# Kernel tuning notes

Hardware: AMD Instinct MI355X
Metric: run time of the kernel (lower is better)

## Reference

```python
import jax, jax.numpy as jnp
import numpy as np

D_MODEL = 1024
HIDDEN = 2048
D_STATE = 16
KERN = 3
BATCH = 2
SEQ = 2048


def _layernorm(x, g, b, eps=1e-5):
    m = jnp.mean(x, axis=-1, keepdims=True)
    v = jnp.var(x, axis=-1, keepdims=True)
    return (x - m) * jax.lax.rsqrt(v + eps) * g + b


def setup_inputs() -> dict:
    key = jax.random.key(0)
    ks = jax.random.split(key, 10)
    w_scale = 0.02  # keep pre-activations in a sane range (mimics trained-net init)
    return {
        "x": jax.random.normal(ks[0], (BATCH, SEQ, D_MODEL), jnp.float32),
        "W_x": jax.random.normal(ks[1], (HIDDEN, D_MODEL), jnp.float32) * w_scale,
        "b_x": jnp.zeros((HIDDEN,), jnp.float32),
        "W_g": jax.random.normal(ks[2], (HIDDEN, D_MODEL), jnp.float32) * w_scale,
        "b_g": jnp.zeros((HIDDEN,), jnp.float32),
        "conv_w": jax.random.normal(ks[3], (HIDDEN, 1, KERN), jnp.float32) * 0.3,
        "conv_b": jnp.zeros((HIDDEN,), jnp.float32),
        "A_raw": jax.random.normal(ks[4], (HIDDEN, D_STATE), jnp.float32),
        "B_ssm": jax.random.normal(ks[5], (HIDDEN, D_STATE), jnp.float32),
        "C_ssm": jax.random.normal(ks[6], (HIDDEN, D_STATE), jnp.float32),
        "W_dt": jax.random.normal(ks[7], (HIDDEN, D_MODEL), jnp.float32) * w_scale,
        "b_dt": jnp.zeros((HIDDEN,), jnp.float32),
        "W_out": jax.random.normal(ks[8], (D_MODEL, HIDDEN), jnp.float32) * w_scale,
        "b_out": jnp.zeros((D_MODEL,), jnp.float32),
        "ln_g": jnp.ones((D_MODEL,), jnp.float32),
        "ln_b": jnp.zeros((D_MODEL,), jnp.float32),
    }


def reference(x, W_x, b_x, W_g, b_g, conv_w, conv_b, A_raw, B_ssm, C_ssm,
              W_dt, b_dt, W_out, b_out, ln_g, ln_b):
    # projections: u, gate
    u = jnp.einsum('bld,hd->blh', x, W_x) + b_x                    # [B,L,H]
    g = jax.nn.sigmoid(jnp.einsum('bld,hd->blh', x, W_g) + b_g)    # [B,L,H]
    # depthwise conv over time (padding = kernel//2, 'same' for odd kernel)
    pad = conv_w.shape[-1] // 2
    h = jax.lax.conv_general_dilated(
        jnp.transpose(u, (0, 2, 1)), conv_w,
        window_strides=(1,), padding=[(pad, pad)],
        feature_group_count=conv_w.shape[0],
        dimension_numbers=('NCH', 'OIH', 'NCH')) + conv_b[None, :, None]
    h = jnp.transpose(h, (0, 2, 1))                                # [B,L,H]
    u = u * g + h * (1.0 - g)
    # time-invariant dt per channel (mean over batch & time, clamped)
    dt = jax.nn.softplus(jnp.einsum('bld,hd->blh', x, W_dt) + b_dt).mean(axis=(0, 1))
    dt = jnp.clip(dt, 1e-3, 2.0)                                   # [H]
    # discretize
    A = -jax.nn.softplus(A_raw)                                    # [H,S]
    A_d = jnp.exp(A * dt[:, None])                                 # [H,S]
    B_d = (A_d - 1.0) / (A + 1e-6) * B_ssm                         # [H,S]
    # selective scan: state s[b,h,k] = A_d*s + B_d*u_t ; y = <s, C>
    Bsz, L, H = u.shape
    S = A_d.shape[1]

    def step(carry, u_t):                                          # u_t: [B,H]
        new = A_d[None] * carry + B_d[None] * u_t[:, :, None]      # [B,H,S]
        y_t = jnp.einsum('bhs,hs->bh', new, C_ssm)
        return new, y_t

    init = jnp.zeros((Bsz, H, S), dtype=u.dtype)
    _, ys = jax.lax.scan(step, init, jnp.transpose(u, (1, 0, 2)))  # ys: [L,B,H]
    y = jnp.transpose(ys, (1, 0, 2))                               # [B,L,H]
    out = jnp.einsum('blh,dh->bld', y, W_out) + b_out
    return _layernorm(x + out, ln_g, ln_b)
```

## Files before the change

### kernel.cpp

```cpp
#include <hip/hip_runtime.h>
#include <math.h>

#define D_MODEL 1024
#define HIDDEN  2048
#define D_STATE 16
#define BATCH   2
#define SEQ     2048
#define NTOK    (BATCH*SEQ)
#define CHUNK   64
#define NCHUNK  (SEQ/CHUNK)

typedef __attribute__((ext_vector_type(8))) short bf16x8;
typedef __attribute__((ext_vector_type(8))) unsigned short ushort8;
typedef __attribute__((ext_vector_type(4))) float f32x4;

#define GLOAD_LDS16(gptr, lptr) \
    __builtin_amdgcn_global_load_lds((const __attribute__((address_space(1))) void*)(gptr), \
                                     (__attribute__((address_space(3))) void*)(lptr), 16, 0, 0)

__device__ __forceinline__ float softplus_f(float x) {
    return fmaxf(x, 0.0f) + log1pf(expf(-fabsf(x)));
}
__device__ __forceinline__ float sigmoid_f(float x) {
    return 1.0f / (1.0f + expf(-x));
}
__device__ __forceinline__ ushort f2bf(float f) {
    unsigned u = __float_as_uint(f);
    unsigned r = (u + 0x7fffu + ((u >> 16) & 1u)) >> 16;
    return (ushort)r;
}
__device__ __forceinline__ float bf2f(ushort u) {
    return __uint_as_float(((unsigned)u) << 16);
}

__global__ __launch_bounds__(256) void cvt_all(
    const float* __restrict__ x, const float* __restrict__ Wx,
    const float* __restrict__ Wg, const float* __restrict__ Wdt,
    const float* __restrict__ Wout, ushort* __restrict__ arena)
{
    int i = blockIdx.x * 256 + threadIdx.x;
    const float* src; int base;
    if      (i < 1048576) { src = x;    base = 0; }
    else if (i < 1572864) { src = Wx;   base = 1048576; }
    else if (i < 2097152) { src = Wg;   base = 1572864; }
    else if (i < 2621440) { src = Wdt;  base = 2097152; }
    else                  { src = Wout; base = 2621440; }
    float4 v = reinterpret_cast<const float4*>(src)[i - base];
    ushort4 o = { f2bf(v.x), f2bf(v.y), f2bf(v.z), f2bf(v.w) };
    reinterpret_cast<ushort4*>(arena)[i] = o;
}

__device__ __forceinline__ void kloop_pipe3(
    const ushort* __restrict__ A, const ushort* __restrict__ B,
    int K, int m0, int n0, ushort* As, ushort* Bs,
    f32x4 (&acc)[4][4], int lane, int w, int wm, int wn)
{
    const int lr   = lane >> 2;
    const int kc   = (lane & 3) * 8;
    const int quad = lane >> 4;
    const int fr   = lane & 15;

    const int slab0 = w * 2;
    const int r0 = slab0 * 16 + lr;
    const int r1 = r0 + 16;
    const size_t ga0 = (size_t)(m0 + r0) * K + kc;
    const size_t ga1 = (size_t)(m0 + r1) * K + kc;
    const size_t gb0 = (size_t)(n0 + r0) * K + kc;
    const size_t gb1 = (size_t)(n0 + r1) * K + kc;

    const int niter = K / 32;
    GLOAD_LDS16(A + ga0,      &As[slab0 * 512]);
    GLOAD_LDS16(A + ga1,      &As[slab0 * 512 + 512]);
    GLOAD_LDS16(B + gb0,      &Bs[slab0 * 512]);
    GLOAD_LDS16(B + gb1,      &Bs[slab0 * 512 + 512]);
    GLOAD_LDS16(A + ga0 + 32, &As[4096 + slab0 * 512]);
    GLOAD_LDS16(A + ga1 + 32, &As[4096 + slab0 * 512 + 512]);
    GLOAD_LDS16(B + gb0 + 32, &Bs[4096 + slab0 * 512]);
    GLOAD_LDS16(B + gb1 + 32, &Bs[4096 + slab0 * 512 + 512]);

    int buf = 0;
    for (int i = 0; i < niter; i++) {
        asm volatile("s_waitcnt vmcnt(4) lgkmcnt(0)" ::: "memory");
        asm volatile("s_barrier" ::: "memory");
        int nb = buf + 2; if (nb >= 3) nb -= 3;
        const size_t koff = (i + 2 < niter) ? (size_t)(i + 2) * 32 : 0;
        GLOAD_LDS16(A + ga0 + koff, &As[nb * 4096 + slab0 * 512]);
        GLOAD_LDS16(A + ga1 + koff, &As[nb * 4096 + slab0 * 512 + 512]);
        GLOAD_LDS16(B + gb0 + koff, &Bs[nb * 4096 + slab0 * 512]);
        GLOAD_LDS16(B + gb1 + koff, &Bs[nb * 4096 + slab0 * 512 + 512]);

        const ushort* as = &As[buf * 4096];
        const ushort* bs = &Bs[buf * 4096];
        bf16x8 af[4], bfv[4];
        #pragma unroll
        for (int t = 0; t < 4; t++) {
            af[t]  = *reinterpret_cast<const bf16x8*>(&as[(wm * 64 + t * 16 + fr) * 32 + quad * 8]);
            bfv[t] = *reinterpret_cast<const bf16x8*>(&bs[(wn * 64 + t * 16 + fr) * 32 + quad * 8]);
        }
        #pragma unroll
        for (int ii = 0; ii < 4; ii++)
            #pragma unroll
            for (int jj = 0; jj < 4; jj++)
                acc[ii][jj] = __builtin_amdgcn_mfma_f32_16x16x32_bf16(af[ii], bfv[jj], acc[ii][jj], 0, 0, 0);
        buf = (buf == 2) ? 0 : buf + 1;
    }
    asm volatile("s_waitcnt vmcnt(0) lgkmcnt(0)" ::: "memory");
    asm volatile("s_barrier" ::: "memory");
}

__global__ __launch_bounds__(256) void proj_gemm_fused(
    const ushort* __restrict__ xbf, const ushort* __restrict__ Wcat,
    const float* __restrict__ b_x, const float* __restrict__ b_g,
    const float* __restrict__ b_dt, ushort* __restrict__ u_out,
    ushort* __restrict__ g_out, float* __restrict__ dt_sum)
{
    __shared__ ushort S[24576];
    ushort* As = S;
    ushort* Bs = S + 12288;
    const int tid = threadIdx.x, lane = tid & 63, w = tid >> 6;
    const int wm = w & 1, wn = w >> 1;
    const int m0 = blockIdx.x * 128, n0 = blockIdx.y * 128;
    const int quad = lane >> 4, fr = lane & 15;

    f32x4 acc[4][4];
    #pragma unroll
    for (int i = 0; i < 4; i++)
        #pragma unroll
        for (int j = 0; j < 4; j++)
            acc[i][j] = (f32x4){0.f, 0.f, 0.f, 0.f};

    kloop_pipe3(xbf, Wcat, D_MODEL, m0, n0, As, Bs, acc, lane, w, wm, wn);

    const int region = n0 >> 11;
    const int ncb = n0 & 2047;

    if (region == 2) {
        #pragma unroll
        for (int j = 0; j < 4; j++) {
            int n = ncb + wn * 64 + j * 16 + fr;
            float bj = b_dt[n];
            float s = 0.f;
            #pragma unroll
            for (int i = 0; i < 4; i++)
                #pragma unroll
                for (int r = 0; r < 4; r++)
                    s += softplus_f(acc[i][j][r] + bj);
            s += __shfl_xor(s, 16);
            s += __shfl_xor(s, 32);
            if (lane < 16) atomicAdd(&dt_sum[n], s);
        }
    } else {
        const float* bias = region ? b_g : b_x;
        ushort* out = region ? g_out : u_out;
        ushort* Cs = S;
        #pragma unroll
        for (int j = 0; j < 4; j++) {
            int col = wn * 64 + j * 16 + fr;
            float bj = bias[ncb + col];
            #pragma unroll
            for (int i = 0; i < 4; i++) {
                int row = wm * 64 + i * 16 + quad * 4;
                #pragma unroll
                for (int r = 0; r < 4; r++) {
                    float v = acc[i][j][r] + bj;
                    if (region) v = sigmoid_f(v);
                    Cs[(row + r) * 128 + col] = f2bf(v);
                }
            }
        }
        __syncthreads();
        #pragma unroll
        for (int k = 0; k < 8; k++) {
            int v = k * 256 + tid;
            int row = v >> 4, c = (v & 15) * 8;
            *reinterpret_cast<ushort8*>(&out[(size_t)(m0 + row) * HIDDEN + ncb + c]) =
                *reinterpret_cast<const ushort8*>(&Cs[v * 8]);
        }
    }
}

__global__ __launch_bounds__(256) void gemm_out(
    const ushort* __restrict__ ybf, const ushort* __restrict__ Wout,
    const float* __restrict__ b_out, const float* __restrict__ x,
    float* __restrict__ resid)
{
    __shared__ ushort S[24576];
    ushort* As = S;
    ushort* Bs = S + 12288;
    const int tid = threadIdx.x, lane = tid & 63, w = tid >> 6;
    const int wm = w & 1, wn = w >> 1;
    const int m0 = blockIdx.x * 128, n0 = blockIdx.y * 128;
    const int quad = lane >> 4, fr = lane & 15;

    f32x4 acc[4][4];
    #pragma unroll
    for (int i = 0; i < 4; i++)
        #pragma unroll
        for (int j = 0; j < 4; j++)
            acc[i][j] = (f32x4){0.f, 0.f, 0.f, 0.f};

    kloop_pipe3(ybf, Wout, HIDDEN, m0, n0, As, Bs, acc, lane, w, wm, wn);

    float* Sf = (float*)S;
    #pragma unroll
    for (int phase = 0; phase < 2; phase++) {
        if (wm == phase) {
            #pragma unroll
            for (int j = 0; j < 4; j++) {
                int col = wn * 64 + j * 16 + fr;
                float bj = b_out[n0 + col];
                #pragma unroll
                for (int i = 0; i < 4; i++) {
                    int row = i * 16 + quad * 4;
                    #pragma unroll
                    for (int r = 0; r < 4; r++)
                        Sf[(row + r) * 128 + col] = acc[i][j][r] + bj;
                }
            }
        }
        __syncthreads();
        #pragma unroll
        for (int k = 0; k < 8; k++) {
            int v = k * 256 + tid;
            int row = v >> 5, c = (v & 31) * 4;
            size_t off = (size_t)(m0 + phase * 64 + row) * D_MODEL + n0 + c;
            float4 xa = *reinterpret_cast<const float4*>(&x[off]);
            float4 cv = *reinterpret_cast<const float4*>(&Sf[v * 4]);
            float4 o = { cv.x + xa.x, cv.y + xa.y, cv.z + xa.z, cv.w + xa.w };
            *reinterpret_cast<float4*>(&resid[off]) = o;
        }
        __syncthreads();
    }
}

__global__ __launch_bounds__(256) void dt_finalize(
    const float* __restrict__ dt_sum, const float* __restrict__ A_raw,
    const float* __restrict__ B_ssm, float* __restrict__ A_d,
    float* __restrict__ B_d, float* __restrict__ A_dL)
{
    int i = blockIdx.x * 256 + threadIdx.x;
    if (i >= HIDDEN * D_STATE) return;
    int h = i >> 4;
    float dt = dt_sum[h] * (1.0f / NTOK);
    dt = fminf(fmaxf(dt, 1e-3f), 2.0f);
    float Av = -softplus_f(A_raw[i]);
    float Ad = expf(Av * dt);
    float Bd = (Ad - 1.0f) / (Av + 1e-6f) * B_ssm[i];
    A_d[i] = Ad;
    B_d[i] = Bd;
    A_dL[i] = expf(Av * dt * CHUNK);
}

__global__ __launch_bounds__(256) void scan_pass1(
    const ushort* __restrict__ u_bf, const ushort* __restrict__ g_bf,
    const float* __restrict__ conv_w, const float* __restrict__ conv_b,
    const float* __restrict__ A_d, const float* __restrict__ B_d,
    const float* __restrict__ C_ssm,
    ushort* __restrict__ ypart, float* __restrict__ states)
{
    int idx = blockIdx.x * 256 + threadIdx.x;
    int h  = idx & (HIDDEN - 1);
    int bc = idx >> 11;
    int c  = bc & (NCHUNK - 1);
    int b  = bc >> 5;
    float Ad[D_STATE], Bd[D_STATE], Cv[D_STATE], st[D_STATE];
    const float4* a4 = reinterpret_cast<const float4*>(A_d  + h * D_STATE);
    const float4* b4 = reinterpret_cast<const float4*>(B_d  + h * D_STATE);
    const float4* c4 = reinterpret_cast<const float4*>(C_ssm + h * D_STATE);
    #pragma unroll
    for (int q = 0; q < 4; q++) {
        float4 av = a4[q], bv = b4[q], cv = c4[q];
        Ad[q*4+0]=av.x; Ad[q*4+1]=av.y; Ad[q*4+2]=av.z; Ad[q*4+3]=av.w;
        Bd[q*4+0]=bv.x; Bd[q*4+1]=bv.y; Bd[q*4+2]=bv.z; Bd[q*4+3]=bv.w;
        Cv[q*4+0]=cv.x; Cv[q*4+1]=cv.y; Cv[q*4+2]=cv.z; Cv[q*4+3]=cv.w;
    }
    #pragma unroll
    for (int s = 0; s < D_STATE; s++) st[s] = 0.f;

    float w0 = conv_w[h * 3 + 0], w1 = conv_w[h * 3 + 1];
    float w2 = conv_w[h * 3 + 2], cb = conv_b[h];
    const int tok0 = c * CHUNK;
    const size_t base = ((size_t)b * SEQ + tok0) * HIDDEN + h;
    float u_prev = (tok0 > 0) ? bf2f(u_bf[base - HIDDEN]) : 0.f;
    float u_cur  = bf2f(u_bf[base]);
    for (int l = 0; l < CHUNK; l++) {
        float u_next = (tok0 + l + 1 < SEQ) ? bf2f(u_bf[base + (size_t)(l + 1) * HIDDEN]) : 0.f;
        float gv = bf2f(g_bf[base + (size_t)l * HIDDEN]);
        float conv = u_prev * w0 + u_cur * w1 + u_next * w2 + cb;
        float uv = u_cur * gv + conv * (1.0f - gv);
        float y0 = 0.f, y1 = 0.f, y2 = 0.f, y3 = 0.f;
        #pragma unroll
        for (int s = 0; s < D_STATE; s += 4) {
            st[s+0] = fmaf(Ad[s+0], st[s+0], Bd[s+0] * uv);
            st[s+1] = fmaf(Ad[s+1], st[s+1], Bd[s+1] * uv);
            st[s+2] = fmaf(Ad[s+2], st[s+2], Bd[s+2] * uv);
            st[s+3] = fmaf(Ad[s+3], st[s+3], Bd[s+3] * uv);
            y0 = fmaf(st[s+0], Cv[s+0], y0);
            y1 = fmaf(st[s+1], Cv[s+1], y1);
            y2 = fmaf(st[s+2], Cv[s+2], y2);
            y3 = fmaf(st[s+3], Cv[s+3], y3);
        }
        ypart[base + (size_t)l * HIDDEN] = f2bf((y0 + y1) + (y2 + y3));
        u_prev = u_cur; u_cur = u_next;
    }
    float4* sp = reinterpret_cast<float4*>(states + ((size_t)bc * HIDDEN + h) * D_STATE);
    #pragma unroll
    for (int q = 0; q < 4; q++)
        sp[q] = (float4){st[q*4+0], st[q*4+1], st[q*4+2], st[q*4+3]};
}

__global__ __launch_bounds__(256) void scan_pass2(
    float* __restrict__ states, const float* __restrict__ A_dL)
{
    int idx = blockIdx.x * 256 + threadIdx.x;
    int s = idx & 15;
    int h = (idx >> 4) & (HIDDEN - 1);
    int b = idx >> 15;
    float aL = A_dL[h * D_STATE + s];
    float carry = 0.f;
    for (int c = 0; c < NCHUNK; c++) {
        size_t addr = (((size_t)(b * NCHUNK + c) * HIDDEN) + h) * D_STATE + s;
        float fin = states[addr];
        states[addr] = carry;
        carry = fmaf(aL, carry, fin);
    }
}

__global__ __launch_bounds__(256) void scan_pass3(
    const ushort* __restrict__ ypart, const float* __restrict__ states,
    const float* __restrict__ A_d, const float* __restrict__ C_ssm,
    ushort* __restrict__ ybf)
{
    int idx = blockIdx.x * 256 + threadIdx.x;
    int h  = idx & (HIDDEN - 1);
    int bc = idx >> 11;
    int c  = bc & (NCHUNK - 1);
    int b  = bc >> 5;
    float Ad[D_STATE], t[D_STATE];
    const float* sp = states + ((size_t)bc * HIDDEN + h) * D_STATE;
    #pragma unroll
    for (int s = 0; s < D_STATE; s++) {
        float a = A_d[h * D_STATE + s];
        Ad[s] = a;
        t[s] = C_ssm[h * D_STATE + s] * a * sp[s];
    }
    const size_t base = ((size_t)b * SEQ + (size_t)c * CHUNK) * HIDDEN + h;
    for (int l = 0; l < CHUNK; l++) {
        float c0 = 0.f, c1 = 0.f;
        #pragma unroll
        for (int s = 0; s < D_STATE; s += 2) {
            c0 += t[s];
            c1 += t[s + 1];
            t[s] *= Ad[s];
            t[s + 1] *= Ad[s + 1];
        }
        ybf[base + (size_t)l * HIDDEN] = f2bf(bf2f(ypart[base + (size_t)l * HIDDEN]) + (c0 + c1));
    }
}

__global__ __launch_bounds__(256) void ln_kernel(
    const float* __restrict__ resid, const float* __restrict__ ln_g,
    const float* __restrict__ ln_b, float* __restrict__ out)
{
    int row = blockIdx.x;
    int tid = threadIdx.x;
    const float4 v = reinterpret_cast<const float4*>(resid + (size_t)row * D_MODEL)[tid];
    float s  = v.x + v.y + v.z + v.w;
    float ss = v.x * v.x + v.y * v.y + v.z * v.z + v.w * v.w;
    #pragma unroll
    for (int off = 32; off > 0; off >>= 1) {
        s  += __shfl_down(s, off);
        ss += __shfl_down(ss, off);
    }
    __shared__ float sbuf[4], ssbuf[4];
    int wid = tid >> 6, lane = tid & 63;
    if (lane == 0) { sbuf[wid] = s; ssbuf[wid] = ss; }
    __syncthreads();
    float tot  = sbuf[0] + sbuf[1] + sbuf[2] + sbuf[3];
    float tot2 = ssbuf[0] + ssbuf[1] + ssbuf[2] + ssbuf[3];
    float mean = tot * (1.0f / D_MODEL);
    float var  = tot2 * (1.0f / D_MODEL) - mean * mean;
    float rstd = rsqrtf(var + 1e-5f);
    const float4 gv = reinterpret_cast<const float4*>(ln_g)[tid];
    const float4 bv = reinterpret_cast<const float4*>(ln_b)[tid];
    float4 o;
    o.x = (v.x - mean) * rstd * gv.x + bv.x;
    o.y = (v.y - mean) * rstd * gv.y + bv.y;
    o.z = (v.z - mean) * rstd * gv.z + bv.z;
    o.w = (v.w - mean) * rstd * gv.w + bv.w;
    reinterpret_cast<float4*>(out + (size_t)row * D_MODEL)[tid] = o;
}

extern "C" void kernel_launch(void* const* d_in, const int* in_sizes, int n_in,
                              void* d_out, int out_size, void* d_ws, size_t ws_size,
                              hipStream_t stream) {
    const float* x      = (const float*)d_in[0];
    const float* W_x    = (const float*)d_in[1];
    const float* b_x    = (const float*)d_in[2];
    const float* W_g    = (const float*)d_in[3];
    const float* b_g    = (const float*)d_in[4];
    const float* conv_w = (const float*)d_in[5];
    const float* conv_b = (const float*)d_in[6];
    const float* A_raw  = (const float*)d_in[7];
    const float* B_ssm  = (const float*)d_in[8];
    const float* C_ssm  = (const float*)d_in[9];
    const float* W_dt   = (const float*)d_in[10];
    const float* b_dt   = (const float*)d_in[11];
    const float* W_out  = (const float*)d_in[12];
    const float* b_out  = (const float*)d_in[13];
    const float* ln_g   = (const float*)d_in[14];
    const float* ln_b   = (const float*)d_in[15];

    char* W = (char*)d_ws;
    ushort* arena   = (ushort*)(W);
    ushort* x_bf    = arena;
    ushort* Wcat    = arena + 4194304;
    ushort* Wout_bf = arena + 10485760;
    ushort* u_bf    = (ushort*)(W + (24ull << 20));
    ushort* g_bf    = (ushort*)(W + (40ull << 20));
    ushort* ypart   = (ushort*)(W + (56ull << 20));
    float*  resid   = (float*)(W + (40ull << 20));
    float*  states  = (float*)(W + (72ull << 20));
    float*  dt_sum  = (float*)(W + (80ull << 20));
    float*  A_d     = (float*)(W + (80ull << 20) + 65536);
    float*  B_d     = (float*)(W + (80ull << 20) + 65536 + 131072);
    float*  A_dL    = (float*)(W + (80ull << 20) + 65536 + 262144);
    ushort* y_bf    = u_bf;

    hipMemsetAsync(dt_sum, 0, HIDDEN * sizeof(float), stream);

    dim3 blk(256);
    cvt_all<<<12288, blk, 0, stream>>>(x, W_x, W_g, W_dt, W_out, arena);

    dim3 grid_proj(NTOK / 128, 3 * HIDDEN / 128);
    proj_gemm_fused<<<grid_proj, blk, 0, stream>>>(x_bf, Wcat, b_x, b_g, b_dt,
                                                   u_bf, g_bf, dt_sum);
    dt_finalize<<<(HIDDEN * D_STATE) / 256, blk, 0, stream>>>(dt_sum, A_raw, B_ssm,
                                                              A_d, B_d, A_dL);
    scan_pass1<<<(BATCH * NCHUNK * HIDDEN) / 256, blk, 0, stream>>>(
        u_bf, g_bf, conv_w, conv_b, A_d, B_d, C_ssm, ypart, states);
    scan_pass2<<<(BATCH * HIDDEN * D_STATE) / 256, blk, 0, stream>>>(states, A_dL);
    scan_pass3<<<(BATCH * NCHUNK * HIDDEN) / 256, blk, 0, stream>>>(ypart, states, A_d,
                                                                    C_ssm, y_bf);
    dim3 grid_out(NTOK / 128, D_MODEL / 128);
    gemm_out<<<grid_out, blk, 0, stream>>>(y_bf, Wout_bf, b_out, x, resid);
    ln_kernel<<<NTOK, blk, 0, stream>>>(resid, ln_g, ln_b, (float*)d_out);
}
```

Baseline: 297.0 us.

## Replace projection GEMM with 256x256-tile, 8-wave kernel with swizzled LDS pipeline

Replaces the 128x128-tile, 4-wave fused projection GEMM with a 256x256-tile, 512-thread kernel. Each wave now accumulates 128x64. The kernel uses a 3-stage global-to-LDS pipeline, XOR-swizzled LDS chunks to avoid bank conflicts, interleaved A/B half-loads between MFMA groups, and s_setprio around the MFMA bursts. The larger tile raises arithmetic intensity and reduces global traffic for the dominant GEMM. In exchange it uses more registers and LDS per block, launches fewer blocks (16x24), and writes the epilogue in two halves through LDS.

```diff
diff --git a/kernel.cpp b/kernel.cpp
--- a/kernel.cpp
+++ b/kernel.cpp
@@ -50,6 +50,141 @@
     reinterpret_cast<ushort4*>(arena)[i] = o;
 }
 
+
+#define PJ_FA(MI) (*reinterpret_cast<const bf16x8*>(&as[(wm * 128 + (MI) * 16 + fr) * 32 + chq * 8]))
+#define PJ_FB(NJ) (*reinterpret_cast<const bf16x8*>(&bs[(wn * 64  + (NJ) * 16 + fr) * 32 + chq * 8]))
+
+#define PJ_MF4(AI, AV) \
+    acc[AI][0] = __builtin_amdgcn_mfma_f32_16x16x32_bf16(AV, b0, acc[AI][0], 0, 0, 0); \
+    acc[AI][1] = __builtin_amdgcn_mfma_f32_16x16x32_bf16(AV, b1, acc[AI][1], 0, 0, 0); \
+    acc[AI][2] = __builtin_amdgcn_mfma_f32_16x16x32_bf16(AV, b2, acc[AI][2], 0, 0, 0); \
+    acc[AI][3] = __builtin_amdgcn_mfma_f32_16x16x32_bf16(AV, b3, acc[AI][3], 0, 0, 0);
+
+__global__ __launch_bounds__(512, 2) void proj_gemm_256(
+    const ushort* __restrict__ xbf, const ushort* __restrict__ Wcat,
+    const float* __restrict__ b_x, const float* __restrict__ b_g,
+    const float* __restrict__ b_dt, ushort* __restrict__ u_out,
+    ushort* __restrict__ g_out, float* __restrict__ dt_sum)
+{
+    __shared__ ushort S[49152];
+    const int tid  = threadIdx.x, lane = tid & 63, w = tid >> 6;
+    const int wm   = w >> 2, wn = w & 3;
+    const int quad = lane >> 4, fr = lane & 15;
+    const int chq  = quad ^ ((fr >> 1) & 3);
+    const int m0   = blockIdx.x * 256, n0 = blockIdx.y * 256;
+
+    const int lr   = lane >> 2;
+    const int qsrc = (lane & 3) ^ ((lane >> 3) & 3);
+    const ushort* sA0 = xbf  + (size_t)(m0 + w * 16 + lr) * 1024 + qsrc * 8;
+    const ushort* sA1 = sA0 + (size_t)128 * 1024;
+    const ushort* sB0 = Wcat + (size_t)(n0 + w * 16 + lr) * 1024 + qsrc * 8;
+    const ushort* sB1 = sB0 + (size_t)128 * 1024;
+
+    f32x4 acc[8][4];
+    #pragma unroll
+    for (int i = 0; i < 8; i++)
+        #pragma unroll
+        for (int j = 0; j < 4; j++)
+            acc[i][j] = (f32x4){0.f, 0.f, 0.f, 0.f};
+
+    GLOAD_LDS16(sA0,      &S[0 * 8192 + w * 512]);
+    GLOAD_LDS16(sA1,      &S[0 * 8192 + 4096 + w * 512]);
+    GLOAD_LDS16(sB0,      &S[24576 + 0 * 8192 + w * 512]);
+    GLOAD_LDS16(sB1,      &S[24576 + 0 * 8192 + 4096 + w * 512]);
+    GLOAD_LDS16(sA0 + 32, &S[1 * 8192 + w * 512]);
+    GLOAD_LDS16(sA1 + 32, &S[1 * 8192 + 4096 + w * 512]);
+    GLOAD_LDS16(sB0 + 32, &S[24576 + 1 * 8192 + w * 512]);
+    GLOAD_LDS16(sB1 + 32, &S[24576 + 1 * 8192 + 4096 + w * 512]);
+    asm volatile("s_waitcnt vmcnt(4)" ::: "memory");
+    asm volatile("s_barrier" ::: "memory");
+
+    int cur = 0;
+    #pragma unroll 1
+    for (int t = 0; t < 32; t++) {
+        const ushort* as = &S[cur * 8192];
+        const ushort* bs = &S[24576 + cur * 8192];
+        int nxt = cur + 2; if (nxt >= 3) nxt -= 3;
+        const size_t koff = (t + 2 < 32) ? (size_t)(t + 2) * 32 : 0;
+
+        bf16x8 b0 = PJ_FB(0), b1 = PJ_FB(1), b2 = PJ_FB(2), b3 = PJ_FB(3);
+        bf16x8 a0 = PJ_FA(0), a1 = PJ_FA(1), a2 = PJ_FA(2), a3 = PJ_FA(3);
+        GLOAD_LDS16(sA0 + koff, &S[nxt * 8192 + w * 512]);
+        GLOAD_LDS16(sA1 + koff, &S[nxt * 8192 + 4096 + w * 512]);
+        asm volatile("s_barrier" ::: "memory");
+        asm volatile("s_waitcnt lgkmcnt(0)" ::: "memory");
+        __builtin_amdgcn_s_setprio(1);
+        PJ_MF4(0, a0) PJ_MF4(1, a1) PJ_MF4(2, a2) PJ_MF4(3, a3)
+        __builtin_amdgcn_s_setprio(0);
+        asm volatile("s_barrier" ::: "memory");
+
+        a0 = PJ_FA(4); a1 = PJ_FA(5); a2 = PJ_FA(6); a3 = PJ_FA(7);
+        GLOAD_LDS16(sB0 + koff, &S[24576 + nxt * 8192 + w * 512]);
+        GLOAD_LDS16(sB1 + koff, &S[24576 + nxt * 8192 + 4096 + w * 512]);
+        asm volatile("s_barrier" ::: "memory");
+        asm volatile("s_waitcnt lgkmcnt(0)" ::: "memory");
+        __builtin_amdgcn_s_setprio(1);
+        PJ_MF4(4, a0) PJ_MF4(5, a1) PJ_MF4(6, a2) PJ_MF4(7, a3)
+        __builtin_amdgcn_s_setprio(0);
+        asm volatile("s_waitcnt vmcnt(4)" ::: "memory");
+        asm volatile("s_barrier" ::: "memory");
+
+        cur++; if (cur >= 3) cur -= 3;
+    }
+    __syncthreads();
+
+    const int region = n0 >> 11;
+    const int ncb = n0 & 2047;
+    if (region == 2) {
+        #pragma unroll
+        for (int j = 0; j < 4; j++) {
+            int col = ncb + wn * 64 + j * 16 + fr;
+            float bj = b_dt[col];
+            float s = 0.f;
+            #pragma unroll
+            for (int i = 0; i < 8; i++)
+                #pragma unroll
+                for (int r = 0; r < 4; r++)
+                    s += softplus_f(acc[i][j][r] + bj);
+            s += __shfl_xor(s, 16);
+            s += __shfl_xor(s, 32);
+            if (lane < 16) atomicAdd(&dt_sum[col], s);
+        }
+    } else {
+        const float* bias = region ? b_g : b_x;
+        ushort* out = region ? g_out : u_out;
+        ushort* Cs = S;
+        #pragma unroll
+        for (int p = 0; p < 2; p++) {
+            if (wm == p) {
+                #pragma unroll
+                for (int j = 0; j < 4; j++) {
+                    int col = wn * 64 + j * 16 + fr;
+                    float bj = bias[ncb + col];
+                    #pragma unroll
+                    for (int i = 0; i < 8; i++) {
+                        int row = i * 16 + quad * 4;
+                        #pragma unroll
+                        for (int r = 0; r < 4; r++) {
+                            float v = acc[i][j][r] + bj;
+                            if (region) v = sigmoid_f(v);
+                            Cs[(row + r) * 256 + col] = f2bf(v);
+                        }
+                    }
+                }
+            }
+            __syncthreads();
+            #pragma unroll
+            for (int k = 0; k < 8; k++) {
+                int v = k * 512 + tid;
+                int row = v >> 5, c = (v & 31) * 8;
+                *reinterpret_cast<ushort8*>(&out[(size_t)(m0 + p * 128 + row) * HIDDEN + ncb + c]) =
+                    *reinterpret_cast<const ushort8*>(&Cs[v * 8]);
+            }
+            __syncthreads();
+        }
+    }
+}
+
 __device__ __forceinline__ void kloop_pipe3(
     const ushort* __restrict__ A, const ushort* __restrict__ B,
     int K, int m0, int n0, ushort* As, ushort* Bs,
@@ -106,77 +241,6 @@
     }
     asm volatile("s_waitcnt vmcnt(0) lgkmcnt(0)" ::: "memory");
     asm volatile("s_barrier" ::: "memory");
-}
-
-__global__ __launch_bounds__(256) void proj_gemm_fused(
-    const ushort* __restrict__ xbf, const ushort* __restrict__ Wcat,
-    const float* __restrict__ b_x, const float* __restrict__ b_g,
-    const float* __restrict__ b_dt, ushort* __restrict__ u_out,
-    ushort* __restrict__ g_out, float* __restrict__ dt_sum)
-{
-    __shared__ ushort S[24576];
-    ushort* As = S;
-    ushort* Bs = S + 12288;
-    const int tid = threadIdx.x, lane = tid & 63, w = tid >> 6;
-    const int wm = w & 1, wn = w >> 1;
-    const int m0 = blockIdx.x * 128, n0 = blockIdx.y * 128;
-    const int quad = lane >> 4, fr = lane & 15;
-
-    f32x4 acc[4][4];
-    #pragma unroll
-    for (int i = 0; i < 4; i++)
-        #pragma unroll
-        for (int j = 0; j < 4; j++)
-            acc[i][j] = (f32x4){0.f, 0.f, 0.f, 0.f};
-
-    kloop_pipe3(xbf, Wcat, D_MODEL, m0, n0, As, Bs, acc, lane, w, wm, wn);
-
-    const int region = n0 >> 11;
-    const int ncb = n0 & 2047;
-
-    if (region == 2) {
-        #pragma unroll
-        for (int j = 0; j < 4; j++) {
-            int n = ncb + wn * 64 + j * 16 + fr;
-            float bj = b_dt[n];
-            float s = 0.f;
-            #pragma unroll
-            for (int i = 0; i < 4; i++)
-                #pragma unroll
-                for (int r = 0; r < 4; r++)
-                    s += softplus_f(acc[i][j][r] + bj);
-            s += __shfl_xor(s, 16);
-            s += __shfl_xor(s, 32);
-            if (lane < 16) atomicAdd(&dt_sum[n], s);
-        }
-    } else {
-        const float* bias = region ? b_g : b_x;
-        ushort* out = region ? g_out : u_out;
-        ushort* Cs = S;
-        #pragma unroll
-        for (int j = 0; j < 4; j++) {
-            int col = wn * 64 + j * 16 + fr;
-            float bj = bias[ncb + col];
-            #pragma unroll
-            for (int i = 0; i < 4; i++) {
-                int row = wm * 64 + i * 16 + quad * 4;
-                #pragma unroll
-                for (int r = 0; r < 4; r++) {
-                    float v = acc[i][j][r] + bj;
-                    if (region) v = sigmoid_f(v);
-                    Cs[(row + r) * 128 + col] = f2bf(v);
-                }
-            }
-        }
-        __syncthreads();
-        #pragma unroll
-        for (int k = 0; k < 8; k++) {
-            int v = k * 256 + tid;
-            int row = v >> 4, c = (v & 15) * 8;
-            *reinterpret_cast<ushort8*>(&out[(size_t)(m0 + row) * HIDDEN + ncb + c]) =
-                *reinterpret_cast<const ushort8*>(&Cs[v * 8]);
-        }
-    }
 }
 
 __global__ __launch_bounds__(256) void gemm_out(
@@ -432,9 +496,9 @@
     dim3 blk(256);
     cvt_all<<<12288, blk, 0, stream>>>(x, W_x, W_g, W_dt, W_out, arena);
 
-    dim3 grid_proj(NTOK / 128, 3 * HIDDEN / 128);
-    proj_gemm_fused<<<grid_proj, blk, 0, stream>>>(x_bf, Wcat, b_x, b_g, b_dt,
-                                                   u_bf, g_bf, dt_sum);
+    dim3 grid_proj(NTOK / 256, 3 * HIDDEN / 256);
+    proj_gemm_256<<<grid_proj, dim3(512), 0, stream>>>(x_bf, Wcat, b_x, b_g, b_dt,
+                                                       u_bf, g_bf, dt_sum);
     dt_finalize<<<(HIDDEN * D_STATE) / 256, blk, 0, stream>>>(dt_sum, A_raw, B_ssm,
                                                               A_d, B_d, A_dL);
     scan_pass1<<<(BATCH * NCHUNK * HIDDEN) / 256, blk, 0, stream>>>(
```

Result: slower. 333.8 us (+12.4%).

## XOR-swizzle LDS tiles and use 64-row tiles for output GEMM

Applied to the files above, without the earlier changes.

Applies an XOR swizzle to the LDS chunk layout in the shared k-loop (both the global-to-LDS load and the fragment reads) to cut LDS bank conflicts on the fragment loads. Replaces the 128x128 output GEMM with a dedicated 64x128 tile kernel that has its own 3-stage pipeline and a single-phase epilogue. This doubles the block count for the out projection, which only had 256 blocks, to fill more CUs. The trade-off is less data reuse per block and more redundant weight loads.

```diff
diff --git a/kernel.cpp b/kernel.cpp
--- a/kernel.cpp
+++ b/kernel.cpp
@@ -56,9 +56,11 @@
     f32x4 (&acc)[4][4], int lane, int w, int wm, int wn)
 {
     const int lr   = lane >> 2;
-    const int kc   = (lane & 3) * 8;
+    const int qsrc = (lane & 3) ^ ((lane >> 3) & 3);
+    const int kc   = qsrc * 8;
     const int quad = lane >> 4;
     const int fr   = lane & 15;
+    const int chq  = quad ^ ((fr >> 1) & 3);
 
     const int slab0 = w * 2;
     const int r0 = slab0 * 16 + lr;
@@ -94,8 +96,8 @@
         bf16x8 af[4], bfv[4];
         #pragma unroll
         for (int t = 0; t < 4; t++) {
-            af[t]  = *reinterpret_cast<const bf16x8*>(&as[(wm * 64 + t * 16 + fr) * 32 + quad * 8]);
-            bfv[t] = *reinterpret_cast<const bf16x8*>(&bs[(wn * 64 + t * 16 + fr) * 32 + quad * 8]);
+            af[t]  = *reinterpret_cast<const bf16x8*>(&as[(wm * 64 + t * 16 + fr) * 32 + chq * 8]);
+            bfv[t] = *reinterpret_cast<const bf16x8*>(&bs[(wn * 64 + t * 16 + fr) * 32 + chq * 8]);
         }
         #pragma unroll
         for (int ii = 0; ii < 4; ii++)
@@ -179,57 +181,92 @@
     }
 }
 
-__global__ __launch_bounds__(256) void gemm_out(
+__global__ __launch_bounds__(256) void gemm_out64(
     const ushort* __restrict__ ybf, const ushort* __restrict__ Wout,
     const float* __restrict__ b_out, const float* __restrict__ x,
     float* __restrict__ resid)
 {
-    __shared__ ushort S[24576];
+    __shared__ ushort S[18432];
     ushort* As = S;
-    ushort* Bs = S + 12288;
+    ushort* Bs = S + 6144;
     const int tid = threadIdx.x, lane = tid & 63, w = tid >> 6;
-    const int wm = w & 1, wn = w >> 1;
-    const int m0 = blockIdx.x * 128, n0 = blockIdx.y * 128;
+    const int m0 = blockIdx.x * 64, n0 = blockIdx.y * 128;
     const int quad = lane >> 4, fr = lane & 15;
-
-    f32x4 acc[4][4];
+    const int lr   = lane >> 2;
+    const int qsrc = (lane & 3) ^ ((lane >> 3) & 3);
+    const int chq  = quad ^ ((fr >> 1) & 3);
+    const int K = HIDDEN;
+
+    const size_t ga  = (size_t)(m0 + w * 16 + lr) * K + qsrc * 8;
+    const size_t gb0 = (size_t)(n0 + w * 16 + lr) * K + qsrc * 8;
+    const size_t gb1 = gb0 + (size_t)64 * K;
+
+    f32x4 acc[4][2];
     #pragma unroll
     for (int i = 0; i < 4; i++)
         #pragma unroll
-        for (int j = 0; j < 4; j++)
+        for (int j = 0; j < 2; j++)
             acc[i][j] = (f32x4){0.f, 0.f, 0.f, 0.f};
 
-    kloop_pipe3(ybf, Wout, HIDDEN, m0, n0, As, Bs, acc, lane, w, wm, wn);
+    GLOAD_LDS16(ybf  + ga,       &As[0 * 2048 + w * 512]);
+    GLOAD_LDS16(Wout + gb0,      &Bs[0 * 4096 + w * 512]);
+    GLOAD_LDS16(Wout + gb1,      &Bs[0 * 4096 + 2048 + w * 512]);
+    GLOAD_LDS16(ybf  + ga + 32,  &As[1 * 2048 + w * 512]);
+    GLOAD_LDS16(Wout + gb0 + 32, &Bs[1 * 4096 + w * 512]);
+    GLOAD_LDS16(Wout + gb1 + 32, &Bs[1 * 4096 + 2048 + w * 512]);
+
+    int buf = 0;
+    for (int t = 0; t < 64; t++) {
+        asm volatile("s_waitcnt vmcnt(3) lgkmcnt(0)" ::: "memory");
+        asm volatile("s_barrier" ::: "memory");
+        int nb = buf + 2; if (nb >= 3) nb -= 3;
+        const size_t koff = (t + 2 < 64) ? (size_t)(t + 2) * 32 : 0;
+        GLOAD_LDS16(ybf  + ga + koff,  &As[nb * 2048 + w * 512]);
+        GLOAD_LDS16(Wout + gb0 + koff, &Bs[nb * 4096 + w * 512]);
+        GLOAD_LDS16(Wout + gb1 + koff, &Bs[nb * 4096 + 2048 + w * 512]);
+
+        const ushort* as = &As[buf * 2048];
+        const ushort* bs = &Bs[buf * 4096];
+        bf16x8 af[4], bfv[2];
+        #pragma unroll
+        for (int mi = 0; mi < 4; mi++)
+            af[mi] = *reinterpret_cast<const bf16x8*>(&as[(mi * 16 + fr) * 32 + chq * 8]);
+        #pragma unroll
+        for (int nj = 0; nj < 2; nj++)
+            bfv[nj] = *reinterpret_cast<const bf16x8*>(&bs[(w * 32 + nj * 16 + fr) * 32 + chq * 8]);
+        #pragma unroll
+        for (int mi = 0; mi < 4; mi++)
+            #pragma unroll
+            for (int nj = 0; nj < 2; nj++)
+                acc[mi][nj] = __builtin_amdgcn_mfma_f32_16x16x32_bf16(af[mi], bfv[nj], acc[mi][nj], 0, 0, 0);
+        buf = (buf == 2) ? 0 : buf + 1;
+    }
+    asm volatile("s_waitcnt vmcnt(0) lgkmcnt(0)" ::: "memory");
+    asm volatile("s_barrier" ::: "memory");
 
     float* Sf = (float*)S;
     #pragma unroll
-    for (int phase = 0; phase < 2; phase++) {
-        if (wm == phase) {
+    for (int nj = 0; nj < 2; nj++) {
+        int col = w * 32 + nj * 16 + fr;
+        float bj = b_out[n0 + col];
+        #pragma unroll
+        for (int mi = 0; mi < 4; mi++) {
+            int row = mi * 16 + quad * 4;
             #pragma unroll
-            for (int j = 0; j < 4; j++) {
-                int col = wn * 64 + j * 16 + fr;
-                float bj = b_out[n0 + col];
-                #pragma unroll
-                for (int i = 0; i < 4; i++) {
-                    int row = i * 16 + quad * 4;
-                    #pragma unroll
-                    for (int r = 0; r < 4; r++)
-                        Sf[(row + r) * 128 + col] = acc[i][j][r] + bj;
-                }
-            }
-        }
-        __syncthreads();
-        #pragma unroll
-        for (int k = 0; k < 8; k++) {
-            int v = k * 256 + tid;
-            int row = v >> 5, c = (v & 31) * 4;
-            size_t off = (size_t)(m0 + phase * 64 + row) * D_MODEL + n0 + c;
-            float4 xa = *reinterpret_cast<const float4*>(&x[off]);
-            float4 cv = *reinterpret_cast<const float4*>(&Sf[v * 4]);
-            float4 o = { cv.x + xa.x, cv.y + xa.y, cv.z + xa.z, cv.w + xa.w };
-            *reinterpret_cast<float4*>(&resid[off]) = o;
-        }
-        __syncthreads();
+            for (int r = 0; r < 4; r++)
+                Sf[(row + r) * 128 + col] = acc[mi][nj][r] + bj;
+        }
+    }
+    __syncthreads();
+    #pragma unroll
+    for (int k = 0; k < 8; k++) {
+        int v = k * 256 + tid;
+        int row = v >> 5, c = (v & 31) * 4;
+        size_t off = (size_t)(m0 + row) * D_MODEL + n0 + c;
+        float4 xa = *reinterpret_cast<const float4*>(&x[off]);
+        float4 cv = *reinterpret_cast<const float4*>(&Sf[v * 4]);
+        float4 o = { cv.x + xa.x, cv.y + xa.y, cv.z + xa.z, cv.w + xa.w };
+        *reinterpret_cast<float4*>(&resid[off]) = o;
     }
 }
 
@@ -442,7 +479,7 @@
     scan_pass2<<<(BATCH * HIDDEN * D_STATE) / 256, blk, 0, stream>>>(states, A_dL);
     scan_pass3<<<(BATCH * NCHUNK * HIDDEN) / 256, blk, 0, stream>>>(ypart, states, A_d,
                                                                     C_ssm, y_bf);
-    dim3 grid_out(NTOK / 128, D_MODEL / 128);
-    gemm_out<<<grid_out, blk, 0, stream>>>(y_bf, Wout_bf, b_out, x, resid);
+    dim3 grid_out(NTOK / 64, D_MODEL / 128);
+    gemm_out64<<<grid_out, blk, 0, stream>>>(y_bf, Wout_bf, b_out, x, resid);
     ln_kernel<<<NTOK, blk, 0, stream>>>(resid, ln_g, ln_b, (float*)d_out);
 }
```

After: 297.5 us. No clear change (+0.2%).
